# Kernel optimization log

Hardware: AMD Instinct MI355X
Metric: run time of the kernel (lower is better)

Reference implementation:

```python
import jax, jax.numpy as jnp
import numpy as np

B = 2
D_MODEL = 256
D_FFN = 1024
N_LEVELS = 4
N_HEADS = 8
N_POINTS = 4
D_HEAD = D_MODEL // N_HEADS
SHAPES = np.array([[128, 128], [64, 64], [32, 32], [16, 16]], dtype=np.int32)  # (H, W) per level
LEN = int(SHAPES.prod(axis=1).sum())  # 21760
EPS = 1e-5


def _layer_norm(x, g, b):
    m = jnp.mean(x, axis=-1, keepdims=True)
    v = jnp.mean(jnp.square(x - m), axis=-1, keepdims=True)
    return (x - m) * jax.lax.rsqrt(v + EPS) * g + b


def _bilinear_gather(v_l, loc, H, W):
    # v_l: [B, H*W, NH, DH]; loc: [B, L, NH, NP, 2] in normalized [0,1] coords (x, y)
    # grid_sample(align_corners=False, padding_mode=zeros) semantics: pixel = loc * size - 0.5
    x = loc[..., 0] * W - 0.5
    y = loc[..., 1] * H - 0.5
    x0 = jnp.floor(x)
    y0 = jnp.floor(y)
    dx = x - x0
    dy = y - y0
    x0i = x0.astype(jnp.int32)
    y0i = y0.astype(jnp.int32)
    b_ix = jnp.arange(v_l.shape[0])[:, None, None, None]
    h_ix = jnp.arange(v_l.shape[2])[None, None, :, None]

    def corner(xi, yi, w):
        valid = (xi >= 0) & (xi < W) & (yi >= 0) & (yi < H)
        idx = jnp.clip(yi, 0, H - 1) * W + jnp.clip(xi, 0, W - 1)
        v = v_l[b_ix, idx, h_ix]  # [B, L, NH, NP, DH]
        return v * (w * valid.astype(v.dtype))[..., None]

    return (corner(x0i, y0i, (1 - dx) * (1 - dy))
            + corner(x0i + 1, y0i, dx * (1 - dy))
            + corner(x0i, y0i + 1, (1 - dx) * dy)
            + corner(x0i + 1, y0i + 1, dx * dy))


def _forward(src, pos, reference_points,
             w_off, b_off, w_attn, b_attn, w_val, b_val, w_out, b_out,
             ln1_g, ln1_b, w1, b1, w2, b2, ln2_g, ln2_b,
             spatial_shapes, level_start_index, padding_mask):
    shapes = np.asarray(spatial_shapes)        # static per-level (H, W)
    starts = np.asarray(level_start_index)     # static level offsets
    Bsz, L, _ = src.shape

    # ---- MSDeformAttn ----
    q = src + pos                              # with_pos_embed
    value = src @ w_val + b_val
    value = jnp.where(padding_mask[..., None], 0.0, value)
    value = value.reshape(Bsz, L, N_HEADS, D_HEAD)

    off = (q @ w_off + b_off).reshape(Bsz, L, N_HEADS, N_LEVELS, N_POINTS, 2)
    attn = (q @ w_attn + b_attn).reshape(Bsz, L, N_HEADS, N_LEVELS * N_POINTS)
    attn = jax.nn.softmax(attn, axis=-1).reshape(Bsz, L, N_HEADS, N_LEVELS, N_POINTS)

    wh = jnp.asarray(shapes[:, ::-1].copy(), dtype=src.dtype)  # [NL, 2] = (W, H)
    loc = reference_points[:, :, None, :, None, :] + off / wh[None, None, None, :, None, :]

    out = jnp.zeros((Bsz, L, N_HEADS, D_HEAD), src.dtype)
    for l in range(N_LEVELS):
        H, W = int(shapes[l, 0]), int(shapes[l, 1])
        s = int(starts[l])
        v_l = value[:, s:s + H * W]                          # [B, H*W, NH, DH]
        sampled = _bilinear_gather(v_l, loc[:, :, :, l], H, W)  # [B, L, NH, NP, DH]
        out = out + (sampled * attn[:, :, :, l][..., None]).sum(axis=3)
    attn_out = out.reshape(Bsz, L, D_MODEL) @ w_out + b_out

    # ---- residual + LN + FFN + residual + LN (dropout = identity in eval) ----
    x = _layer_norm(src + attn_out, ln1_g, ln1_b)
    ffn = jax.nn.relu(x @ w1 + b1) @ w2 + b2
    return _layer_norm(x + ffn, ln2_g, ln2_b)


def setup_inputs() -> dict:
    key = jax.random.key(0)
    ks = jax.random.split(key, 16)
    s = 0.02
    n_off = N_HEADS * N_LEVELS * N_POINTS
    level_start = np.concatenate([[0], SHAPES.prod(axis=1).cumsum()[:-1]]).astype(np.int32)
    return {
        "src": jax.random.normal(ks[0], (B, LEN, D_MODEL), jnp.float32),
        "pos": jax.random.normal(ks[1], (B, LEN, D_MODEL), jnp.float32),
        "reference_points": jax.random.uniform(ks[2], (B, LEN, N_LEVELS, 2), jnp.float32),
        "spatial_shapes": jnp.asarray(SHAPES),
        "level_start_index": jnp.asarray(level_start),
        "padding_mask": jnp.zeros((B, LEN), jnp.bool_),
        "w_off": jax.random.normal(ks[3], (D_MODEL, n_off * 2), jnp.float32) * s,
        "b_off": jax.random.normal(ks[4], (n_off * 2,), jnp.float32) * 0.5,
        "w_attn": jax.random.normal(ks[5], (D_MODEL, n_off), jnp.float32) * s,
        "b_attn": jnp.zeros((n_off,), jnp.float32),
        "w_val": jax.random.normal(ks[6], (D_MODEL, D_MODEL), jnp.float32) * s,
        "b_val": jnp.zeros((D_MODEL,), jnp.float32),
        "w_out": jax.random.normal(ks[7], (D_MODEL, D_MODEL), jnp.float32) * s,
        "b_out": jnp.zeros((D_MODEL,), jnp.float32),
        "ln1_g": jnp.ones((D_MODEL,), jnp.float32),
        "ln1_b": jnp.zeros((D_MODEL,), jnp.float32),
        "w1": jax.random.normal(ks[8], (D_MODEL, D_FFN), jnp.float32) * s,
        "b1": jnp.zeros((D_FFN,), jnp.float32),
        "w2": jax.random.normal(ks[9], (D_FFN, D_MODEL), jnp.float32) * s,
        "b2": jnp.zeros((D_MODEL,), jnp.float32),
        "ln2_g": jnp.ones((D_MODEL,), jnp.float32),
        "ln2_b": jnp.zeros((D_MODEL,), jnp.float32),
    }


def reference(src, pos, reference_points, spatial_shapes, level_start_index, padding_mask,
              w_off, b_off, w_attn, b_attn, w_val, b_val, w_out, b_out,
              ln1_g, ln1_b, w1, b1, w2, b2, ln2_g, ln2_b):
    return _forward(src, pos, reference_points,
                    w_off, b_off, w_attn, b_attn, w_val, b_val, w_out, b_out,
                    ln1_g, ln1_b, w1, b1, w2, b2, ln2_g, ln2_b,
                    spatial_shapes, level_start_index, padding_mask)
```

## Files before the change

### kernel.cpp

```cpp
#include <hip/hip_runtime.h>
#include <hip/hip_bf16.h>

#define BSZ      2
#define LTOK     21760
#define NTOK     (BSZ * LTOK)
#define DMODEL   256
#define DFFN     1024

typedef __attribute__((ext_vector_type(8))) short short8;
typedef __attribute__((ext_vector_type(4))) float f32x4;

__device__ __forceinline__ unsigned short f2bf(float x) {
    __hip_bfloat16 h = __float2bfloat16(x);
    return *reinterpret_cast<unsigned short*>(&h);
}
__device__ __forceinline__ float bf2f(unsigned short u) {
    union { unsigned int i; float f; } c; c.i = ((unsigned int)u) << 16; return c.f;
}
__device__ __forceinline__ float bflo(unsigned int u) {
    union { unsigned int i; float f; } c; c.i = u << 16; return c.f;
}
__device__ __forceinline__ float bfhi(unsigned int u) {
    union { unsigned int i; float f; } c; c.i = u & 0xffff0000u; return c.f;
}

#define TM 128
#define TN 256
#define TBK 32
#define EBS 264

__global__ __launch_bounds__(256, 2) void gemm_mfma(
    const unsigned short* __restrict__ A,
    const unsigned short* __restrict__ Bt, const float* __restrict__ bias,
    unsigned short* __restrict__ Cb,
    int M, int N, int K, int relu, int cmode,
    const unsigned char* __restrict__ mask)
{
    __shared__ __align__(16) unsigned short smem[TM * TBK + TN * TBK];
    unsigned short* sA = smem;
    unsigned short* sB = smem + TM * TBK;

    const int tid  = threadIdx.x;
    const int lane = tid & 63;
    const int wave = tid >> 6;
    const int wm = wave >> 1, wn = wave & 1;

    const int bm = blockIdx.y * TM;
    const int bn = blockIdx.x * TN;

    const int sr = tid >> 6;
    const int fr = lane & 15;
    const int fk = (lane >> 4) * 8;

    f32x4 acc[4][8];
    #pragma unroll
    for (int i = 0; i < 4; ++i)
        #pragma unroll
        for (int j = 0; j < 8; ++j)
            acc[i][j] = (f32x4){0.f, 0.f, 0.f, 0.f};

    for (int k0 = 0; k0 < K; k0 += TBK) {
        #pragma unroll
        for (int rr = 0; rr < 2; ++rr) {
            const int s = sr + rr * 4;
            const size_t grow = (size_t)(bm + s * 16 + fr);
            *(uint4*)&sA[s * 512 + lane * 8] = *(const uint4*)(A + grow * K + k0 + fk);
        }
        #pragma unroll
        for (int rr = 0; rr < 4; ++rr) {
            const int s = sr + rr * 4;
            int gn = bn + s * 16 + fr;
            gn = min(gn, N - 1);
            *(uint4*)&sB[s * 512 + lane * 8] = *(const uint4*)(Bt + (size_t)gn * K + k0 + fk);
        }
        __syncthreads();

        short8 af[4], bfr[8];
        #pragma unroll
        for (int i = 0; i < 4; ++i)
            af[i] = *(const short8*)&sA[(wm * 4 + i) * 512 + lane * 8];
        #pragma unroll
        for (int j = 0; j < 8; ++j)
            bfr[j] = *(const short8*)&sB[(wn * 8 + j) * 512 + lane * 8];
        #pragma unroll
        for (int i = 0; i < 4; ++i)
            #pragma unroll
            for (int j = 0; j < 8; ++j)
                acc[i][j] = __builtin_amdgcn_mfma_f32_16x16x32_bf16(
                    af[i], bfr[j], acc[i][j], 0, 0, 0);
        __syncthreads();
    }

    const int r0 = (lane >> 4) * 4;
    const int c0 = lane & 15;
    unsigned short* eb = smem;

    #pragma unroll
    for (int i = 0; i < 4; ++i) {
        if (i) __syncthreads();
        #pragma unroll
        for (int j = 0; j < 8; ++j) {
            const int col = bn + wn * 128 + j * 16 + c0;
            const float bj = (col < N) ? bias[col] : 0.f;
            #pragma unroll
            for (int r = 0; r < 4; ++r) {
                const int row = bm + wm * 64 + i * 16 + r0 + r;
                float v = acc[i][j][r] + bj;
                if (relu) v = fmaxf(v, 0.f);
                if (mask && mask[row]) v = 0.f;
                eb[(wm * 16 + r0 + r) * EBS + wn * 128 + j * 16 + c0] = f2bf(v);
            }
        }
        __syncthreads();
        #pragma unroll
        for (int qq = 0; qq < 4; ++qq) {
            const int q  = tid + qq * 256;
            const int rl = q >> 5;
            const int ch = q & 31;
            const int grow = bm + (rl >> 4) * 64 + i * 16 + (rl & 15);
            const int colb = bn + ch * 8;
            if (colb < N) {
                const uint4 val = *(const uint4*)&eb[rl * EBS + ch * 8];
                if (cmode == 1) {
                    const int bb   = grow >= LTOK;
                    const int srow = grow - bb * LTOK;
                    const int hcol = ch >> 2;
                    const int d    = (ch & 3) * 8;
                    *(uint4*)&Cb[((size_t)(bb * 8 + hcol) * LTOK + srow) * 32 + d] = val;
                } else {
                    *(uint4*)&Cb[(size_t)grow * N + colb] = val;
                }
            }
        }
    }
}

__global__ __launch_bounds__(256) void prepass(
    const float* __restrict__ src, const float* __restrict__ pos,
    unsigned short* __restrict__ sb, unsigned short* __restrict__ qs)
{
    const size_t i = ((size_t)blockIdx.x * 256 + threadIdx.x) * 4;
    const float4 s = *(const float4*)(src + i);
    const float4 p = *(const float4*)(pos + i);
    ushort4 us, uq;
    us.x = f2bf(s.x); us.y = f2bf(s.y); us.z = f2bf(s.z); us.w = f2bf(s.w);
    uq.x = f2bf(s.x + p.x); uq.y = f2bf(s.y + p.y);
    uq.z = f2bf(s.z + p.z); uq.w = f2bf(s.w + p.w);
    *(ushort4*)(sb + i) = us;
    *(ushort4*)(qs + i) = uq;
}

__global__ void transpose_all(
    const float* __restrict__ w_val, const float* __restrict__ w_off,
    const float* __restrict__ w_att, const float* __restrict__ w_out,
    const float* __restrict__ w1,    const float* __restrict__ w2,
    const float* __restrict__ b_off, const float* __restrict__ b_att,
    unsigned short* __restrict__ wvalT, unsigned short* __restrict__ woaT,
    unsigned short* __restrict__ woutT, unsigned short* __restrict__ w1T,
    unsigned short* __restrict__ w2T,   float* __restrict__ bcat)
{
    const int blk = blockIdx.x;
    const int tx = threadIdx.x, ty = threadIdx.y;
    if (blk == 736) {
        const int t = ty * 32 + tx;
        bcat[t] = (t < 256) ? b_off[t] : b_att[t - 256];
        if (t + 256 < 384) bcat[t + 256] = b_att[t];
        return;
    }
    const float* W; unsigned short* Wt; int K, N, base;
    if      (blk < 64)  { W = w_val; Wt = wvalT;           K = 256;  N = 256;  base = 0;   }
    else if (blk < 128) { W = w_off; Wt = woaT;            K = 256;  N = 256;  base = 64;  }
    else if (blk < 160) { W = w_att; Wt = woaT + 256*256;  K = 256;  N = 128;  base = 128; }
    else if (blk < 224) { W = w_out; Wt = woutT;           K = 256;  N = 256;  base = 160; }
    else if (blk < 480) { W = w1;    Wt = w1T;             K = 256;  N = 1024; base = 224; }
    else                { W = w2;    Wt = w2T;             K = 1024; N = 256;  base = 480; }
    const int local = blk - base;
    const int kb = local % (K / 32);
    const int nb = local / (K / 32);
    const int k0 = kb * 32, n0 = nb * 32;

    __shared__ float t[32][33];
    #pragma unroll
    for (int i = 0; i < 32; i += 8)
        t[ty + i][tx] = W[(size_t)(k0 + ty + i) * N + n0 + tx];
    __syncthreads();
    #pragma unroll
    for (int i = 0; i < 32; i += 8)
        Wt[(size_t)(n0 + ty + i) * K + k0 + tx] = f2bf(t[tx][ty + i]);
}

__global__ __launch_bounds__(256) void sample_kernel(
    const unsigned short* __restrict__ vT, const unsigned short* __restrict__ qp,
    const float* __restrict__ ref,
    const int* __restrict__ sshapes, const int* __restrict__ lstart,
    unsigned short* __restrict__ samp)
{
    __shared__ __align__(16) int   s_o[256][4];
    __shared__ __align__(16) float s_w[256][4];

    const int blk   = blockIdx.x;
    const int plane = blk & 15;
    const int chunk = blk >> 4;
    const int b = plane >> 3;
    const int h = plane & 7;
    const int s0 = chunk * 16;
    const int t = threadIdx.x;

    {
        const int tl = t >> 4;
        const int p  = t & 15;
        const int l  = p >> 2;
        const int pp = p & 3;
        const int H = sshapes[2 * l], W = sshapes[2 * l + 1];
        const float Wf = (float)W, Hf = (float)H;
        const size_t tok = (size_t)(b * LTOK + s0 + tl);

        const float ox = bf2f(qp[tok * 384 + h * 32 + l * 8 + pp * 2 + 0]);
        const float oy = bf2f(qp[tok * 384 + h * 32 + l * 8 + pp * 2 + 1]);
        const float rx = ref[tok * 8 + l * 2 + 0];
        const float ry = ref[tok * 8 + l * 2 + 1];

        const float x = (rx + ox / Wf) * Wf - 0.5f;
        const float y = (ry + oy / Hf) * Hf - 0.5f;
        const float x0 = floorf(x), y0 = floorf(y);
        const float dx = x - x0, dy = y - y0;
        const int x0i = (int)x0, y0i = (int)y0;
        const int s = lstart[l];

        const float a = bf2f(qp[tok * 384 + 256 + h * 16 + p]);
        float mx = a;
        #pragma unroll
        for (int m = 8; m; m >>= 1) mx = fmaxf(mx, __shfl_xor(mx, m, 16));
        const float e = __expf(a - mx);
        float ssum = e;
        #pragma unroll
        for (int m = 8; m; m >>= 1) ssum += __shfl_xor(ssum, m, 16);
        const float prob = e / ssum;

        const float cw[4] = {(1.f - dx) * (1.f - dy), dx * (1.f - dy),
                             (1.f - dx) * dy,         dx * dy};
        const int cx[4] = {x0i, x0i + 1, x0i,     x0i + 1};
        const int cy[4] = {y0i, y0i,     y0i + 1, y0i + 1};
        int4   o4;
        float4 w4;
        #pragma unroll
        for (int c = 0; c < 4; ++c) {
            const bool valid = (cx[c] >= 0) & (cx[c] < W) & (cy[c] >= 0) & (cy[c] < H);
            const int xi = min(max(cx[c], 0), W - 1);
            const int yi = min(max(cy[c], 0), H - 1);
            ((int*)&o4)[c]   = (s + yi * W + xi) * 64;
            ((float*)&w4)[c] = valid ? cw[c] * prob : 0.f;
        }
        const int r = p * 16 + tl;
        *(int4*)&s_o[r][0]   = o4;
        *(float4*)&s_w[r][0] = w4;
    }
    __syncthreads();

    const int tl = t >> 4;
    const int dp = t & 15;
    const char* vp = (const char*)(vT + (size_t)plane * LTOK * 32) + dp * 4;
    float acc0 = 0.f, acc1 = 0.f;
    #pragma unroll
    for (int p = 0; p < 16; ++p) {
        const int r = p * 16 + tl;
        const int4   o4 = *(const int4*)&s_o[r][0];
        const float4 w4 = *(const float4*)&s_w[r][0];
        const unsigned int u0 = *(const unsigned int*)(vp + o4.x);
        const unsigned int u1 = *(const unsigned int*)(vp + o4.y);
        const unsigned int u2 = *(const unsigned int*)(vp + o4.z);
        const unsigned int u3 = *(const unsigned int*)(vp + o4.w);
        acc0 = fmaf(w4.x, bflo(u0), acc0); acc1 = fmaf(w4.x, bfhi(u0), acc1);
        acc0 = fmaf(w4.y, bflo(u1), acc0); acc1 = fmaf(w4.y, bfhi(u1), acc1);
        acc0 = fmaf(w4.z, bflo(u2), acc0); acc1 = fmaf(w4.z, bfhi(u2), acc1);
        acc0 = fmaf(w4.w, bflo(u3), acc0); acc1 = fmaf(w4.w, bfhi(u3), acc1);
    }
    const unsigned int o = (unsigned)f2bf(acc0) | ((unsigned)f2bf(acc1) << 16);
    *(unsigned int*)(samp + (size_t)(b * LTOK + s0 + tl) * 256 + h * 32 + dp * 2) = o;
}

__global__ __launch_bounds__(256) void ln_kernel(
    const unsigned short* __restrict__ a, const unsigned short* __restrict__ b,
    const float* __restrict__ g, const float* __restrict__ be,
    float* __restrict__ outF, unsigned short* __restrict__ outB)
{
    const int wid  = threadIdx.x >> 6;
    const int lane = threadIdx.x & 63;
    const int tok  = blockIdx.x * 4 + wid;
    const size_t base = (size_t)tok * 256 + lane * 4;

    const ushort4 ua = *(const ushort4*)(a + base);
    const ushort4 ub = *(const ushort4*)(b + base);
    float4 v;
    v.x = bf2f(ua.x) + bf2f(ub.x);
    v.y = bf2f(ua.y) + bf2f(ub.y);
    v.z = bf2f(ua.z) + bf2f(ub.z);
    v.w = bf2f(ua.w) + bf2f(ub.w);

    float s  = v.x + v.y + v.z + v.w;
    float sq = v.x * v.x + v.y * v.y + v.z * v.z + v.w * v.w;
    #pragma unroll
    for (int m = 32; m; m >>= 1) {
        s  += __shfl_xor(s, m, 64);
        sq += __shfl_xor(sq, m, 64);
    }
    const float mean = s * (1.f / 256.f);
    const float var  = sq * (1.f / 256.f) - mean * mean;
    const float rs   = rsqrtf(var + 1e-5f);

    const float4 g4 = *(const float4*)(g + lane * 4);
    const float4 b4 = *(const float4*)(be + lane * 4);
    float4 o;
    o.x = (v.x - mean) * rs * g4.x + b4.x;
    o.y = (v.y - mean) * rs * g4.y + b4.y;
    o.z = (v.z - mean) * rs * g4.z + b4.z;
    o.w = (v.w - mean) * rs * g4.w + b4.w;
    if (outF) *(float4*)(outF + base) = o;
    if (outB) {
        ushort4 u;
        u.x = f2bf(o.x); u.y = f2bf(o.y); u.z = f2bf(o.z); u.w = f2bf(o.w);
        *(ushort4*)(outB + base) = u;
    }
}

extern "C" void kernel_launch(void* const* d_in, const int* in_sizes, int n_in,
                              void* d_out, int out_size, void* d_ws, size_t ws_size,
                              hipStream_t stream)
{
    const float* src   = (const float*)d_in[0];
    const float* pos   = (const float*)d_in[1];
    const float* ref   = (const float*)d_in[2];
    const int*   sshap = (const int*)d_in[3];
    const int*   lstrt = (const int*)d_in[4];
    const unsigned char* mask = (const unsigned char*)d_in[5];
    const float* w_off = (const float*)d_in[6];
    const float* b_off = (const float*)d_in[7];
    const float* w_att = (const float*)d_in[8];
    const float* b_att = (const float*)d_in[9];
    const float* w_val = (const float*)d_in[10];
    const float* b_val = (const float*)d_in[11];
    const float* w_out = (const float*)d_in[12];
    const float* b_out = (const float*)d_in[13];
    const float* ln1g  = (const float*)d_in[14];
    const float* ln1b  = (const float*)d_in[15];
    const float* w1    = (const float*)d_in[16];
    const float* b1    = (const float*)d_in[17];
    const float* w2    = (const float*)d_in[18];
    const float* b2    = (const float*)d_in[19];
    const float* ln2g  = (const float*)d_in[20];
    const float* ln2b  = (const float*)d_in[21];
    float* out = (float*)d_out;

    const size_t HSZ = (size_t)NTOK * 256 * 2;
    char* w = (char*)d_ws;
    unsigned short* qs     = (unsigned short*)w;
    unsigned short* samp16 = (unsigned short*)w;
    unsigned short* qpb    = (unsigned short*)(w + HSZ);
    unsigned short* vT     = (unsigned short*)(w + HSZ * 5 / 2);
    unsigned short* aof16  = (unsigned short*)(w + HSZ * 7 / 2);
    unsigned short* hidb   = (unsigned short*)w;
    unsigned short* sb     = (unsigned short*)(w + HSZ * 9 / 2);
    unsigned short* ffb    = sb;
    unsigned short* xb     = (unsigned short*)(w + HSZ * 11 / 2);
    char* wreg = w + HSZ * 13 / 2;
    unsigned short* wvalT  = (unsigned short*)wreg;
    unsigned short* woaT   = wvalT + 256 * 256;
    unsigned short* woutT  = woaT + 384 * 256;
    unsigned short* w1T    = woutT + 256 * 256;
    unsigned short* w2T    = w1T + 1024 * 256;
    float*          bcat   = (float*)(w2T + 256 * 1024);

    const dim3 blk(256);

    prepass<<<dim3(NTOK / 4), blk, 0, stream>>>(src, pos, sb, qs);

    transpose_all<<<dim3(737), dim3(32, 8), 0, stream>>>(
        w_val, w_off, w_att, w_out, w1, w2, b_off, b_att,
        wvalT, woaT, woutT, w1T, w2T, bcat);

    gemm_mfma<<<dim3(1, NTOK / TM), blk, 0, stream>>>(
        sb, wvalT, b_val, vT, NTOK, 256, 256, 0, 1, mask);

    gemm_mfma<<<dim3(2, NTOK / TM), blk, 0, stream>>>(
        qs, woaT, bcat, qpb, NTOK, 384, 256, 0, 0, nullptr);

    sample_kernel<<<dim3(16 * (LTOK / 16)), blk, 0, stream>>>(
        vT, qpb, ref, sshap, lstrt, samp16);

    gemm_mfma<<<dim3(1, NTOK / TM), blk, 0, stream>>>(
        samp16, woutT, b_out, aof16, NTOK, 256, 256, 0, 0, nullptr);

    ln_kernel<<<dim3(NTOK / 4), blk, 0, stream>>>(
        sb, aof16, ln1g, ln1b, nullptr, xb);

    gemm_mfma<<<dim3(4, NTOK / TM), blk, 0, stream>>>(
        xb, w1T, b1, hidb, NTOK, DFFN, 256, 1, 0, nullptr);

    gemm_mfma<<<dim3(1, NTOK / TM), blk, 0, stream>>>(
        hidb, w2T, b2, ffb, NTOK, 256, DFFN, 0, 0, nullptr);

    ln_kernel<<<dim3(NTOK / 4), blk, 0, stream>>>(
        xb, ffb, ln2g, ln2b, out, nullptr);
}
```

Baseline: 482.2 us.

## Fuse residual+LayerNorm into GEMM epilogues and merge value/offset projections

Merges the value projection and offset/attention projection GEMMs into a single launch with a 3-wide grid. It also fuses the residual add and LayerNorm into the epilogues of the output-projection and FFN2 GEMMs, removing two standalone LN kernels and their intermediate bf16 buffers. The aim is fewer launches and less global traffic for intermediates. The cost is a heavier epilogue with extra syncs and strided residual reads inside the GEMM blocks.

```diff
diff --git a/kernel.cpp b/kernel.cpp
--- a/kernel.cpp
+++ b/kernel.cpp
@@ -29,35 +29,17 @@
 #define TBK 32
 #define EBS 264
 
-__global__ __launch_bounds__(256, 2) void gemm_mfma(
+__device__ __forceinline__ void gemm_core(
     const unsigned short* __restrict__ A,
-    const unsigned short* __restrict__ Bt, const float* __restrict__ bias,
-    unsigned short* __restrict__ Cb,
-    int M, int N, int K, int relu, int cmode,
-    const unsigned char* __restrict__ mask)
-{
-    __shared__ __align__(16) unsigned short smem[TM * TBK + TN * TBK];
-    unsigned short* sA = smem;
-    unsigned short* sB = smem + TM * TBK;
-
-    const int tid  = threadIdx.x;
-    const int lane = tid & 63;
-    const int wave = tid >> 6;
-    const int wm = wave >> 1, wn = wave & 1;
-
-    const int bm = blockIdx.y * TM;
-    const int bn = blockIdx.x * TN;
-
+    const unsigned short* __restrict__ Bt,
+    unsigned short* sA, unsigned short* sB,
+    int bm, int bn, int N, int K,
+    int tid, int lane, int wm, int wn,
+    f32x4 acc[4][8])
+{
     const int sr = tid >> 6;
     const int fr = lane & 15;
     const int fk = (lane >> 4) * 8;
-
-    f32x4 acc[4][8];
-    #pragma unroll
-    for (int i = 0; i < 4; ++i)
-        #pragma unroll
-        for (int j = 0; j < 8; ++j)
-            acc[i][j] = (f32x4){0.f, 0.f, 0.f, 0.f};
 
     for (int k0 = 0; k0 < K; k0 += TBK) {
         #pragma unroll
@@ -90,11 +72,98 @@
                     af[i], bfr[j], acc[i][j], 0, 0, 0);
         __syncthreads();
     }
+}
+
+__global__ __launch_bounds__(256, 2) void gemm_mfma(
+    const unsigned short* __restrict__ A,
+    const unsigned short* __restrict__ Bt, const float* __restrict__ bias,
+    unsigned short* __restrict__ Cb,
+    int M, int N, int K, int relu)
+{
+    __shared__ __align__(16) unsigned short smem[TM * TBK + TN * TBK];
+    const int tid  = threadIdx.x;
+    const int lane = tid & 63;
+    const int wave = tid >> 6;
+    const int wm = wave >> 1, wn = wave & 1;
+    const int bm = blockIdx.y * TM;
+    const int bn = blockIdx.x * TN;
+
+    f32x4 acc[4][8];
+    #pragma unroll
+    for (int i = 0; i < 4; ++i)
+        #pragma unroll
+        for (int j = 0; j < 8; ++j)
+            acc[i][j] = (f32x4){0.f, 0.f, 0.f, 0.f};
+
+    gemm_core(A, Bt, smem, smem + TM * TBK, bm, bn, N, K, tid, lane, wm, wn, acc);
 
     const int r0 = (lane >> 4) * 4;
     const int c0 = lane & 15;
     unsigned short* eb = smem;
-
+    #pragma unroll
+    for (int i = 0; i < 4; ++i) {
+        if (i) __syncthreads();
+        #pragma unroll
+        for (int j = 0; j < 8; ++j) {
+            const int col = bn + wn * 128 + j * 16 + c0;
+            const float bj = (col < N) ? bias[col] : 0.f;
+            #pragma unroll
+            for (int r = 0; r < 4; ++r) {
+                float v = acc[i][j][r] + bj;
+                if (relu) v = fmaxf(v, 0.f);
+                eb[(wm * 16 + r0 + r) * EBS + wn * 128 + j * 16 + c0] = f2bf(v);
+            }
+        }
+        __syncthreads();
+        #pragma unroll
+        for (int qq = 0; qq < 4; ++qq) {
+            const int q  = tid + qq * 256;
+            const int rl = q >> 5;
+            const int ch = q & 31;
+            const int grow = bm + (rl >> 4) * 64 + i * 16 + (rl & 15);
+            const int colb = bn + ch * 8;
+            if (colb < N)
+                *(uint4*)&Cb[(size_t)grow * N + colb] =
+                    *(const uint4*)&eb[rl * EBS + ch * 8];
+        }
+    }
+}
+
+__global__ __launch_bounds__(256, 2) void gemm_proj(
+    const unsigned short* __restrict__ A0, const unsigned short* __restrict__ B0,
+    const float* __restrict__ bias0, unsigned short* __restrict__ C0,
+    const unsigned char* __restrict__ mask,
+    const unsigned short* __restrict__ A1, const unsigned short* __restrict__ B1,
+    const float* __restrict__ bias1, unsigned short* __restrict__ C1)
+{
+    __shared__ __align__(16) unsigned short smem[TM * TBK + TN * TBK];
+    const int tid  = threadIdx.x;
+    const int lane = tid & 63;
+    const int wave = tid >> 6;
+    const int wm = wave >> 1, wn = wave & 1;
+    const int bm = blockIdx.y * TM;
+    const int bx = blockIdx.x;
+
+    const int isv = (bx == 0);
+    const unsigned short* A    = isv ? A0 : A1;
+    const unsigned short* Bt   = isv ? B0 : B1;
+    const float*          bias = isv ? bias0 : bias1;
+    const int N  = isv ? 256 : 384;
+    const int bn = isv ? 0 : (bx - 1) * 256;
+    const int K  = 256;
+
+    f32x4 acc[4][8];
+    #pragma unroll
+    for (int i = 0; i < 4; ++i)
+        #pragma unroll
+        for (int j = 0; j < 8; ++j)
+            acc[i][j] = (f32x4){0.f, 0.f, 0.f, 0.f};
+
+    gemm_core(A, Bt, smem, smem + TM * TBK, bm, bn, N, K, tid, lane, wm, wn, acc);
+
+    const int r0 = (lane >> 4) * 4;
+    const int c0 = lane & 15;
+    unsigned short* eb = smem;
     #pragma unroll
     for (int i = 0; i < 4; ++i) {
         if (i) __syncthreads();
@@ -106,8 +175,7 @@
             for (int r = 0; r < 4; ++r) {
                 const int row = bm + wm * 64 + i * 16 + r0 + r;
                 float v = acc[i][j][r] + bj;
-                if (relu) v = fmaxf(v, 0.f);
-                if (mask && mask[row]) v = 0.f;
+                if (isv && mask[row]) v = 0.f;
                 eb[(wm * 16 + r0 + r) * EBS + wn * 128 + j * 16 + c0] = f2bf(v);
             }
         }
@@ -121,17 +189,119 @@
             const int colb = bn + ch * 8;
             if (colb < N) {
                 const uint4 val = *(const uint4*)&eb[rl * EBS + ch * 8];
-                if (cmode == 1) {
+                if (isv) {
                     const int bb   = grow >= LTOK;
                     const int srow = grow - bb * LTOK;
                     const int hcol = ch >> 2;
                     const int d    = (ch & 3) * 8;
-                    *(uint4*)&Cb[((size_t)(bb * 8 + hcol) * LTOK + srow) * 32 + d] = val;
+                    *(uint4*)&C0[((size_t)(bb * 8 + hcol) * LTOK + srow) * 32 + d] = val;
                 } else {
-                    *(uint4*)&Cb[(size_t)grow * N + colb] = val;
+                    *(uint4*)&C1[(size_t)grow * 384 + colb] = val;
                 }
             }
         }
+    }
+}
+
+__global__ __launch_bounds__(256, 2) void gemm_ln(
+    const unsigned short* __restrict__ A,
+    const unsigned short* __restrict__ Bt, const float* __restrict__ bias,
+    const unsigned short* __restrict__ resid,
+    const float* __restrict__ g, const float* __restrict__ be,
+    float* __restrict__ outF, unsigned short* __restrict__ outB, int K)
+{
+    __shared__ __align__(16) unsigned short smem[TM * TBK + TN * TBK];
+    const int tid  = threadIdx.x;
+    const int lane = tid & 63;
+    const int wave = tid >> 6;
+    const int wm = wave >> 1, wn = wave & 1;
+    const int bm = blockIdx.y * TM;
+
+    f32x4 acc[4][8];
+    #pragma unroll
+    for (int i = 0; i < 4; ++i)
+        #pragma unroll
+        for (int j = 0; j < 8; ++j)
+            acc[i][j] = (f32x4){0.f, 0.f, 0.f, 0.f};
+
+    gemm_core(A, Bt, smem, smem + TM * TBK, bm, 0, 256, K, tid, lane, wm, wn, acc);
+
+    const int r0 = (lane >> 4) * 4;
+    const int c0 = lane & 15;
+    unsigned short* eb = smem;
+
+    #pragma unroll
+    for (int i = 0; i < 4; ++i) {
+        if (i) __syncthreads();
+        #pragma unroll
+        for (int j = 0; j < 8; ++j) {
+            const int col = wn * 128 + j * 16 + c0;
+            const float bj = bias[col];
+            #pragma unroll
+            for (int r = 0; r < 4; ++r)
+                eb[(wm * 16 + r0 + r) * EBS + col] = f2bf(acc[i][j][r] + bj);
+        }
+        __syncthreads();
+
+        const int row = tid >> 3;
+        const int l   = tid & 7;
+        const int grow = bm + (row >> 4) * 64 + i * 16 + (row & 15);
+        const unsigned short* rr = resid + (size_t)grow * 256 + l * 32;
+
+        float s = 0.f, sq = 0.f;
+        #pragma unroll
+        for (int k = 0; k < 4; ++k) {
+            const uint4 e = *(const uint4*)&eb[row * EBS + l * 32 + k * 8];
+            const uint4 rv = *(const uint4*)(rr + k * 8);
+            const unsigned int eu[4] = {e.x, e.y, e.z, e.w};
+            const unsigned int ru[4] = {rv.x, rv.y, rv.z, rv.w};
+            #pragma unroll
+            for (int q = 0; q < 4; ++q) {
+                const float v0 = bflo(eu[q]) + bflo(ru[q]);
+                const float v1 = bfhi(eu[q]) + bfhi(ru[q]);
+                s += v0 + v1;
+                sq += v0 * v0 + v1 * v1;
+            }
+        }
+        #pragma unroll
+        for (int m = 4; m; m >>= 1) {
+            s  += __shfl_xor(s, m, 8);
+            sq += __shfl_xor(sq, m, 8);
+        }
+        const float mean = s * (1.f / 256.f);
+        const float var  = sq * (1.f / 256.f) - mean * mean;
+        const float rs   = rsqrtf(var + 1e-5f);
+
+        #pragma unroll
+        for (int k = 0; k < 4; ++k) {
+            const int col = l * 32 + k * 8;
+            const uint4 e = *(const uint4*)&eb[row * EBS + col];
+            const uint4 rv = *(const uint4*)(rr + k * 8);
+            const unsigned int eu[4] = {e.x, e.y, e.z, e.w};
+            const unsigned int ru[4] = {rv.x, rv.y, rv.z, rv.w};
+            float o[8];
+            #pragma unroll
+            for (int q = 0; q < 4; ++q) {
+                const float g0 = g[col + q * 2],     b0 = be[col + q * 2];
+                const float g1 = g[col + q * 2 + 1], b1 = be[col + q * 2 + 1];
+                o[q * 2]     = (bflo(eu[q]) + bflo(ru[q]) - mean) * rs * g0 + b0;
+                o[q * 2 + 1] = (bfhi(eu[q]) + bfhi(ru[q]) - mean) * rs * g1 + b1;
+            }
+            if (outB) {
+                uint4 pk;
+                pk.x = (unsigned)f2bf(o[0]) | ((unsigned)f2bf(o[1]) << 16);
+                pk.y = (unsigned)f2bf(o[2]) | ((unsigned)f2bf(o[3]) << 16);
+                pk.z = (unsigned)f2bf(o[4]) | ((unsigned)f2bf(o[5]) << 16);
+                pk.w = (unsigned)f2bf(o[6]) | ((unsigned)f2bf(o[7]) << 16);
+                *(uint4*)(outB + (size_t)grow * 256 + col) = pk;
+            } else {
+                float4 f0 = make_float4(o[0], o[1], o[2], o[3]);
+                float4 f1 = make_float4(o[4], o[5], o[6], o[7]);
+                *(float4*)(outF + (size_t)grow * 256 + col) = f0;
+                *(float4*)(outF + (size_t)grow * 256 + col + 4) = f1;
+            }
+        }
+        __syncthreads();
     }
 }
 
@@ -277,50 +447,6 @@
     }
     const unsigned int o = (unsigned)f2bf(acc0) | ((unsigned)f2bf(acc1) << 16);
     *(unsigned int*)(samp + (size_t)(b * LTOK + s0 + tl) * 256 + h * 32 + dp * 2) = o;
-}
-
-__global__ __launch_bounds__(256) void ln_kernel(
-    const unsigned short* __restrict__ a, const unsigned short* __restrict__ b,
-    const float* __restrict__ g, const float* __restrict__ be,
-    float* __restrict__ outF, unsigned short* __restrict__ outB)
-{
-    const int wid  = threadIdx.x >> 6;
-    const int lane = threadIdx.x & 63;
-    const int tok  = blockIdx.x * 4 + wid;
-    const size_t base = (size_t)tok * 256 + lane * 4;
-
-    const ushort4 ua = *(const ushort4*)(a + base);
-    const ushort4 ub = *(const ushort4*)(b + base);
-    float4 v;
-    v.x = bf2f(ua.x) + bf2f(ub.x);
-    v.y = bf2f(ua.y) + bf2f(ub.y);
-    v.z = bf2f(ua.z) + bf2f(ub.z);
-    v.w = bf2f(ua.w) + bf2f(ub.w);
-
-    float s  = v.x + v.y + v.z + v.w;
-    float sq = v.x * v.x + v.y * v.y + v.z * v.z + v.w * v.w;
-    #pragma unroll
-    for (int m = 32; m; m >>= 1) {
-        s  += __shfl_xor(s, m, 64);
-        sq += __shfl_xor(sq, m, 64);
-    }
-    const float mean = s * (1.f / 256.f);
-    const float var  = sq * (1.f / 256.f) - mean * mean;
-    const float rs   = rsqrtf(var + 1e-5f);
-
-    const float4 g4 = *(const float4*)(g + lane * 4);
-    const float4 b4 = *(const float4*)(be + lane * 4);
-    float4 o;
-    o.x = (v.x - mean) * rs * g4.x + b4.x;
-    o.y = (v.y - mean) * rs * g4.y + b4.y;
-    o.z = (v.z - mean) * rs * g4.z + b4.z;
-    o.w = (v.w - mean) * rs * g4.w + b4.w;
-    if (outF) *(float4*)(outF + base) = o;
-    if (outB) {
-        ushort4 u;
-        u.x = f2bf(o.x); u.y = f2bf(o.y); u.z = f2bf(o.z); u.w = f2bf(o.w);
-        *(ushort4*)(outB + base) = u;
-    }
 }
 
 extern "C" void kernel_launch(void* const* d_in, const int* in_sizes, int n_in,
@@ -357,10 +483,8 @@
     unsigned short* samp16 = (unsigned short*)w;
     unsigned short* qpb    = (unsigned short*)(w + HSZ);
     unsigned short* vT     = (unsigned short*)(w + HSZ * 5 / 2);
-    unsigned short* aof16  = (unsigned short*)(w + HSZ * 7 / 2);
     unsigned short* hidb   = (unsigned short*)w;
     unsigned short* sb     = (unsigned short*)(w + HSZ * 9 / 2);
-    unsigned short* ffb    = sb;
     unsigned short* xb     = (unsigned short*)(w + HSZ * 11 / 2);
     char* wreg = w + HSZ * 13 / 2;
     unsigned short* wvalT  = (unsigned short*)wreg;
@@ -378,27 +502,18 @@
         w_val, w_off, w_att, w_out, w1, w2, b_off, b_att,
         wvalT, woaT, woutT, w1T, w2T, bcat);
 
-    gemm_mfma<<<dim3(1, NTOK / TM), blk, 0, stream>>>(
-        sb, wvalT, b_val, vT, NTOK, 256, 256, 0, 1, mask);
-
-    gemm_mfma<<<dim3(2, NTOK / TM), blk, 0, stream>>>(
-        qs, woaT, bcat, qpb, NTOK, 384, 256, 0, 0, nullptr);
+    gemm_proj<<<dim3(3, NTOK / TM), blk, 0, stream>>>(
+        sb, wvalT, b_val, vT, mask, qs, woaT, bcat, qpb);
 
     sample_kernel<<<dim3(16 * (LTOK / 16)), blk, 0, stream>>>(
         vT, qpb, ref, sshap, lstrt, samp16);
 
-    gemm_mfma<<<dim3(1, NTOK / TM), blk, 0, stream>>>(
-        samp16, woutT, b_out, aof16, NTOK, 256, 256, 0, 0, nullptr);
-
-    ln_kernel<<<dim3(NTOK / 4), blk, 0, stream>>>(
-        sb, aof16, ln1g, ln1b, nullptr, xb);
+    gemm_ln<<<dim3(1, NTOK / TM), blk, 0, stream>>>(
+        samp16, woutT, b_out, sb, ln1g, ln1b, nullptr, xb, 256);
 
     gemm_mfma<<<dim3(4, NTOK / TM), blk, 0, stream>>>(
-        xb, w1T, b1, hidb, NTOK, DFFN, 256, 1, 0, nullptr);
-
-    gemm_mfma<<<dim3(1, NTOK / TM), blk, 0, stream>>>(
-        hidb, w2T, b2, ffb, NTOK, 256, DFFN, 0, 0, nullptr);
-
-    ln_kernel<<<dim3(NTOK / 4), blk, 0, stream>>>(
-        xb, ffb, ln2g, ln2b, out, nullptr);
-}
+        xb, w1T, b1, hidb, NTOK, DFFN, 256, 1);
+
+    gemm_ln<<<dim3(1, NTOK / TM), blk, 0, stream>>>(
+        hidb, w2T, b2, xb, ln2g, ln2b, out, nullptr, DFFN);
+}
```

Result: no change. 481.7 us (-0.1%).
